# Optimization experiments

Measured on AMD Instinct MI355X. Metric: run time of the kernel, lower is better.

Reference implementation:

```python
import jax, jax.numpy as jnp
import numpy as np

NUM_ITERATIONS = 3
NUM_SLOTS = 8
SLOT_SIZE = 256
MLP_HIDDEN = 512
EPSILON = 1e-8
LN_EPS = 1e-5


def _ln(x, w, b):
    m = jnp.mean(x, axis=-1, keepdims=True)
    v = jnp.var(x, axis=-1, keepdims=True)
    return (x - m) * jax.lax.rsqrt(v + LN_EPS) * w + b


def _gru_cell(x, h, w_ih, w_hh, b_ih, b_hh):
    # torch.nn.GRUCell semantics; gates ordered [r, z, n]
    gi = x @ w_ih.T + b_ih
    gh = h @ w_hh.T + b_hh
    ir, iz, inn = jnp.split(gi, 3, axis=-1)
    hr, hz, hn = jnp.split(gh, 3, axis=-1)
    r = jax.nn.sigmoid(ir + hr)
    z = jax.nn.sigmoid(iz + hz)
    n = jnp.tanh(inn + r * hn)
    return (1.0 - z) * n + z * h


def setup_inputs() -> dict:
    key = jax.random.key(0)
    ks = jax.random.split(key, 12)
    D, H = SLOT_SIZE, MLP_HIDDEN
    s = 0.02
    return {
        "inputs": jax.random.normal(ks[0], (64, 4096, D), dtype=jnp.float32),
        "noise": jax.random.normal(ks[1], (64, NUM_SLOTS, D), dtype=jnp.float32),
        "ln_in_w": jnp.ones((D,), jnp.float32), "ln_in_b": jnp.zeros((D,), jnp.float32),
        "ln_slots_w": jnp.ones((D,), jnp.float32), "ln_slots_b": jnp.zeros((D,), jnp.float32),
        "ln_mlp_w": jnp.ones((D,), jnp.float32), "ln_mlp_b": jnp.zeros((D,), jnp.float32),
        "slots_mu": jax.random.normal(ks[2], (1, 1, D), jnp.float32) * s,
        "slots_log_sigma": jnp.zeros((1, 1, D), jnp.float32),
        "Wq": jax.random.normal(ks[3], (D, D), jnp.float32) * s,
        "Wk": jax.random.normal(ks[4], (D, D), jnp.float32) * s,
        "Wv": jax.random.normal(ks[5], (D, D), jnp.float32) * s,
        "gru_w_ih": jax.random.normal(ks[6], (3 * D, D), jnp.float32) * s,
        "gru_w_hh": jax.random.normal(ks[7], (3 * D, D), jnp.float32) * s,
        "gru_b_ih": jnp.zeros((3 * D,), jnp.float32),
        "gru_b_hh": jnp.zeros((3 * D,), jnp.float32),
        "mlp_w1": jax.random.normal(ks[8], (H, D), jnp.float32) * s,
        "mlp_b1": jnp.zeros((H,), jnp.float32),
        "mlp_w2": jax.random.normal(ks[9], (D, H), jnp.float32) * s,
        "mlp_b2": jnp.zeros((D,), jnp.float32),
    }


def reference(inputs, noise, ln_in_w, ln_in_b, ln_slots_w, ln_slots_b, ln_mlp_w, ln_mlp_b,
              slots_mu, slots_log_sigma, Wq, Wk, Wv,
              gru_w_ih, gru_w_hh, gru_b_ih, gru_b_hh,
              mlp_w1, mlp_b1, mlp_w2, mlp_b2):
    B, N, D = inputs.shape
    S = NUM_SLOTS
    x = _ln(inputs, ln_in_w, ln_in_b)            # [B,N,D]
    k = x @ Wk.T                                  # [B,N,D]
    v = x @ Wv.T                                  # [B,N,D]
    slots = slots_mu + jnp.exp(slots_log_sigma) * noise   # [B,S,D]
    scale = D ** (-0.5)
    for _ in range(NUM_ITERATIONS):
        slots_prev = slots
        s_n = _ln(slots, ln_slots_w, ln_slots_b)
        q = (s_n @ Wq.T) * scale                  # [B,S,D]
        attn_logits = jnp.einsum('bnd,bsd->bns', k, q)
        attn = jax.nn.softmax(attn_logits, axis=-1) + EPSILON
        attn = attn / jnp.sum(attn, axis=-2, keepdims=True)   # renorm over inputs
        updates = jnp.einsum('bns,bnd->bsd', attn, v)          # [B,S,D]
        slots = _gru_cell(updates.reshape(-1, D), slots_prev.reshape(-1, D),
                          gru_w_ih, gru_w_hh, gru_b_ih, gru_b_hh).reshape(B, S, D)
        h = jax.nn.relu(_ln(slots, ln_mlp_w, ln_mlp_b) @ mlp_w1.T + mlp_b1)
        slots = slots + (h @ mlp_w2.T + mlp_b2)
    return slots
```

## Files before the change

kernel.cpp:

```cpp
#include <hip/hip_runtime.h>

#define CB 64
#define CN 4096
#define CD 256
#define CS 8
#define CH 512

typedef __bf16 bf16_t;
typedef bf16_t bf16x8 __attribute__((ext_vector_type(8)));
typedef float f32x4 __attribute__((ext_vector_type(4)));

__device__ __forceinline__ unsigned short f2bf(float f){
  unsigned int u = __builtin_bit_cast(unsigned int, f);
  u += 0x7FFFu + ((u >> 16) & 1u);
  return (unsigned short)(u >> 16);
}

__device__ __forceinline__ f32x4 mfma16(bf16x8 a, bf16x8 b, f32x4 c){
  return __builtin_amdgcn_mfma_f32_16x16x32_bf16(a, b, c, 0, 0, 0);
}

__device__ __forceinline__ void gl_lds16(const void* g, void* l){
  __builtin_amdgcn_global_load_lds(
      (const __attribute__((address_space(1))) unsigned int*)g,
      (__attribute__((address_space(3))) unsigned int*)l, 16, 0, 0);
}

__global__ __launch_bounds__(256) void k_ln(const float* __restrict__ in,
    const float* __restrict__ gw, const float* __restrict__ gb,
    unsigned short* __restrict__ x){
  int blk = blockIdx.x;
  int b = blk >> 6, nt = blk & 63;
  int wv = threadIdx.x >> 6, l = threadIdx.x & 63;
  const float* base = in + ((size_t)b*CN + (size_t)nt*64) * CD;
  unsigned short* xb = x + ((size_t)b*CN + (size_t)nt*64) * CD;
  float4 w4 = *(const float4*)(gw + 4*l);
  float4 b4 = *(const float4*)(gb + 4*l);
  for(int i = 0; i < 16; i++){
    int r = wv*16 + i;
    float4 v = *(const float4*)(base + (size_t)r*CD + 4*l);
    float s1 = v.x + v.y + v.z + v.w;
    float s2 = v.x*v.x + v.y*v.y + v.z*v.z + v.w*v.w;
    #pragma unroll
    for(int m = 1; m < 64; m <<= 1){ s1 += __shfl_xor(s1, m); s2 += __shfl_xor(s2, m); }
    float mean = s1 * (1.0f/CD);
    float var  = fmaxf(s2 * (1.0f/CD) - mean*mean, 0.0f);
    float rstd = rsqrtf(var + 1e-5f);
    float y0 = (v.x - mean)*rstd*w4.x + b4.x;
    float y1 = (v.y - mean)*rstd*w4.y + b4.y;
    float y2 = (v.z - mean)*rstd*w4.z + b4.z;
    float y3 = (v.w - mean)*rstd*w4.w + b4.w;
    uint2 p;
    p.x = (unsigned)f2bf(y0) | ((unsigned)f2bf(y1) << 16);
    p.y = (unsigned)f2bf(y2) | ((unsigned)f2bf(y3) << 16);
    *(uint2*)(xb + (size_t)r*CD + 4*l) = p;
  }
}

__global__ __launch_bounds__(256) void k_setup(
    const float* __restrict__ Wq, const float* __restrict__ Wk,
    const float* __restrict__ wih, const float* __restrict__ Wv,
    const float* __restrict__ whh, const float* __restrict__ w1,
    const float* __restrict__ w2, const float* __restrict__ noise,
    const float* __restrict__ mu, const float* __restrict__ lsig,
    unsigned short* __restrict__ M1T, unsigned short* __restrict__ Mih_bf,
    unsigned short* __restrict__ Whh_bf, unsigned short* __restrict__ w1_bf,
    unsigned short* __restrict__ w2_bf, float* __restrict__ slots){
  int bid = blockIdx.x, tid = threadIdx.x;
  if(bid < 256){
    int ep = bid, e = tid;
    float acc = 0.0f;
    for(int d = 0; d < 256; d++) acc = fmaf(Wq[(size_t)d*256 + e], Wk[(size_t)d*256 + ep], acc);
    M1T[(size_t)ep*256 + e] = f2bf(acc * 0.0625f);
  } else if(bid < 1024){
    int j = bid - 256, e = tid;
    float acc = 0.0f;
    for(int d = 0; d < 256; d++) acc = fmaf(wih[(size_t)j*256 + d], Wv[(size_t)d*256 + e], acc);
    Mih_bf[(size_t)j*256 + e] = f2bf(acc);
  } else if(bid < 1792){
    int idx = (bid - 1024)*256 + tid;
    Whh_bf[idx] = f2bf(whh[idx]);
  } else if(bid < 2304){
    int idx = (bid - 1792)*256 + tid;
    w1_bf[idx] = f2bf(w1[idx]);
  } else if(bid < 2816){
    int idx = (bid - 2304)*256 + tid;
    w2_bf[idx] = f2bf(w2[idx]);
  } else {
    int idx = (bid - 2816)*256 + tid;
    int d = idx & 255;
    slots[idx] = mu[d] + __expf(lsig[d]) * noise[idx];
  }
}

__global__ __launch_bounds__(256) void k_qt(const float* __restrict__ slots,
    const float* __restrict__ lw, const float* __restrict__ lb,
    const unsigned short* __restrict__ M1T, unsigned short* __restrict__ qt,
    float* __restrict__ U, float* __restrict__ den){
  __shared__ unsigned short sn[16*264];
  int b = blockIdx.x;
  int tid = threadIdx.x;
  float4 z4 = {0.f, 0.f, 0.f, 0.f};
  float* Ub = U + (size_t)b*CS*CD;
  *(float4*)(Ub + tid*8)     = z4;
  *(float4*)(Ub + tid*8 + 4) = z4;
  if(tid < CS) den[b*CS + tid] = 0.0f;

  int wv = tid >> 6, l = tid & 63;
  int lm = l & 15, lg = l >> 4;
  float4 w4 = *(const float4*)(lw + 4*l);
  float4 b4 = *(const float4*)(lb + 4*l);
  for(int i = 0; i < 2; i++){
    int r = wv*2 + i;
    float4 v = *(const float4*)(slots + ((size_t)b*CS + r)*CD + 4*l);
    float s1 = v.x + v.y + v.z + v.w;
    float s2 = v.x*v.x + v.y*v.y + v.z*v.z + v.w*v.w;
    #pragma unroll
    for(int m = 1; m < 64; m <<= 1){ s1 += __shfl_xor(s1, m); s2 += __shfl_xor(s2, m); }
    float mean = s1 * (1.0f/CD);
    float var  = fmaxf(s2 * (1.0f/CD) - mean*mean, 0.0f);
    float rstd = rsqrtf(var + 1e-5f);
    float y0 = (v.x - mean)*rstd*w4.x + b4.x;
    float y1 = (v.y - mean)*rstd*w4.y + b4.y;
    float y2 = (v.z - mean)*rstd*w4.z + b4.z;
    float y3 = (v.w - mean)*rstd*w4.w + b4.w;
    uint2 p;
    p.x = (unsigned)f2bf(y0) | ((unsigned)f2bf(y1) << 16);
    p.y = (unsigned)f2bf(y2) | ((unsigned)f2bf(y3) << 16);
    *(uint2*)(&sn[r*264 + 4*l]) = p;
    uint2 zz; zz.x = 0u; zz.y = 0u;
    *(uint2*)(&sn[(r+8)*264 + 4*l]) = zz;
  }
  __syncthreads();
  bf16x8 af[8];
  #pragma unroll
  for(int k = 0; k < 8; k++) af[k] = *(const bf16x8*)(&sn[lm*264 + k*32 + lg*8]);
  #pragma unroll
  for(int ntile = 0; ntile < 4; ntile++){
    int ep = wv*64 + ntile*16 + lm;
    f32x4 acc = {0.f, 0.f, 0.f, 0.f};
    const unsigned short* mrow = M1T + (size_t)ep*CD;
    #pragma unroll
    for(int k = 0; k < 8; k++){
      bf16x8 bf = *(const bf16x8*)(mrow + k*32 + lg*8);
      acc = mfma16(af[k], bf, acc);
    }
    #pragma unroll
    for(int reg = 0; reg < 4; reg++){
      int s = lg*4 + reg;
      qt[((size_t)b*16 + s)*CD + ep] = f2bf(acc[reg]);
    }
  }
}

__global__ __launch_bounds__(256) void k_attn(const unsigned short* __restrict__ x,
    const unsigned short* __restrict__ qt, float* __restrict__ U, float* __restrict__ den){
  __shared__ unsigned short xt[64*256];
  __shared__ unsigned short pt[16*72];
  int b = blockIdx.x >> 4, chunk = blockIdx.x & 15;
  int wv = threadIdx.x >> 6, l = threadIdx.x & 63;
  int lm = l & 15, lg = l >> 4;

  bf16x8 qb[8];
  const unsigned short* qrow = qt + ((size_t)b*16 + lm)*CD;
  #pragma unroll
  for(int k = 0; k < 8; k++) qb[k] = *(const bf16x8*)(qrow + k*32 + lg*8);

  f32x4 uacc[4];
  #pragma unroll
  for(int nt = 0; nt < 4; nt++){ f32x4 z = {0.f,0.f,0.f,0.f}; uacc[nt] = z; }
  float dacc = 0.0f;

  const unsigned short* xbatch = x + (size_t)b*CN*CD + (size_t)chunk*256*CD;

  for(int t = 0; t < 4; t++){
    const unsigned short* xtile = xbatch + (size_t)t*64*CD;
    __syncthreads();
    #pragma unroll
    for(int k2 = 0; k2 < 8; k2++){
      int r0 = wv*16 + k2*2;
      int row = r0 + (l >> 5);
      int c = l & 31;
      int f = (row ^ (row >> 3)) & 7;
      const unsigned short* g = xtile + (size_t)row*CD + (size_t)(c ^ f)*8;
      gl_lds16(g, &xt[r0*CD]);
    }
    __syncthreads();

    f32x4 c4 = {0.f, 0.f, 0.f, 0.f};
    int rowl = wv*16 + lm;
    int f1 = (rowl ^ (rowl >> 3)) & 7;
    #pragma unroll
    for(int k = 0; k < 8; k++){
      int cc = (k*4 + lg) ^ f1;
      bf16x8 a = *(const bf16x8*)(&xt[rowl*256 + cc*8]);
      c4 = mfma16(a, qb[k], c4);
    }
    float pv[4];
    #pragma unroll
    for(int reg = 0; reg < 4; reg++){
      float v = (lm < 8) ? c4[reg] : -1e30f;
      float mx = v;
      #pragma unroll
      for(int m = 1; m < 16; m <<= 1) mx = fmaxf(mx, __shfl_xor(mx, m));
      float e = __expf(v - mx);
      float s = e;
      #pragma unroll
      for(int m = 1; m < 16; m <<= 1) s += __shfl_xor(s, m);
      float p = (lm < 8) ? (e/s + 1e-8f) : 0.0f;
      dacc += p;
      pv[reg] = p;
    }
    int rbase = wv*16 + lg*4;
    unsigned int p01 = (unsigned)f2bf(pv[0]) | ((unsigned)f2bf(pv[1]) << 16);
    unsigned int p23 = (unsigned)f2bf(pv[2]) | ((unsigned)f2bf(pv[3]) << 16);
    *(unsigned int*)(&pt[lm*72 + rbase])     = p01;
    *(unsigned int*)(&pt[lm*72 + rbase + 2]) = p23;
    __syncthreads();

    #pragma unroll
    for(int ks = 0; ks < 2; ks++){
      bf16x8 a = *(const bf16x8*)(&pt[lm*72 + ks*32 + lg*8]);
      int rb = ks*32 + lg*8;
      #pragma unroll
      for(int nt = 0; nt < 4; nt++){
        int e = wv*64 + nt*16 + lm;
        bf16x8 bfr;
        #pragma unroll
        for(int j = 0; j < 8; j++){
          int row2 = rb + j;
          int f2 = (row2 ^ (row2 >> 3)) & 7;
          int cidx = (e >> 3) ^ f2;
          unsigned short tv = xt[row2*256 + cidx*8 + (e & 7)];
          bfr[j] = __builtin_bit_cast(bf16_t, tv);
        }
        uacc[nt] = mfma16(a, bfr, uacc[nt]);
      }
    }
  }

  dacc += __shfl_xor(dacc, 16);
  dacc += __shfl_xor(dacc, 32);
  if(l < 8) atomicAdd(&den[b*CS + l], dacc);
  if(lg < 2){
    #pragma unroll
    for(int nt = 0; nt < 4; nt++){
      #pragma unroll
      for(int reg = 0; reg < 4; reg++){
        int s = lg*4 + reg;
        atomicAdd(&U[((size_t)b*CS + s)*CD + wv*64 + nt*16 + lm], uacc[nt][reg]);
      }
    }
  }
}

__global__ __launch_bounds__(256) void k_update(
    const float* __restrict__ U, const float* slots,
    const float* __restrict__ den,
    const unsigned short* __restrict__ Mih, const unsigned short* __restrict__ Whh,
    const unsigned short* __restrict__ w1b, const unsigned short* __restrict__ w2b,
    const unsigned short* __restrict__ M1T,
    const float* __restrict__ bih, const float* __restrict__ bhh,
    const float* __restrict__ lmw, const float* __restrict__ lmb,
    const float* __restrict__ b1, const float* __restrict__ b2,
    const float* __restrict__ lsw, const float* __restrict__ lsb,
    float* out, unsigned short* __restrict__ qt,
    float* __restrict__ Uz, float* __restrict__ denz, int last){
  __shared__ unsigned short A1[16*264];
  __shared__ unsigned short SBf[16*264];
  __shared__ unsigned short A3[16*520];
  __shared__ float G1[8*777];
  __shared__ float G2[8*777];
  __shared__ float Hh[8*257];
  __shared__ float SN[8*257];
  int b = blockIdx.x, tid = threadIdx.x;
  int l = tid & 63, lm = l & 15, lg = l >> 4;
  int wv = tid >> 6;

  for(int i = tid; i < 8*264; i += 256){ A1[8*264 + i] = 0; SBf[8*264 + i] = 0; }
  for(int i = tid; i < 8*520; i += 256) A3[8*520 + i] = 0;
  {
    int r = tid >> 5, c = (tid & 31)*8;
    const float* Ur = U + ((size_t)b*CS + r)*CD + c;
    float4 a0 = *(const float4*)Ur, a1 = *(const float4*)(Ur + 4);
    uint4 pk;
    pk.x = (unsigned)f2bf(a0.x) | ((unsigned)f2bf(a0.y) << 16);
    pk.y = (unsigned)f2bf(a0.z) | ((unsigned)f2bf(a0.w) << 16);
    pk.z = (unsigned)f2bf(a1.x) | ((unsigned)f2bf(a1.y) << 16);
    pk.w = (unsigned)f2bf(a1.z) | ((unsigned)f2bf(a1.w) << 16);
    *(uint4*)(&A1[r*264 + c]) = pk;
    const float* Sr = slots + ((size_t)b*CS + r)*CD + c;
    a0 = *(const float4*)Sr; a1 = *(const float4*)(Sr + 4);
    pk.x = (unsigned)f2bf(a0.x) | ((unsigned)f2bf(a0.y) << 16);
    pk.y = (unsigned)f2bf(a0.z) | ((unsigned)f2bf(a0.w) << 16);
    pk.z = (unsigned)f2bf(a1.x) | ((unsigned)f2bf(a1.y) << 16);
    pk.w = (unsigned)f2bf(a1.z) | ((unsigned)f2bf(a1.w) << 16);
    *(uint4*)(&SBf[r*264 + c]) = pk;
  }
  __syncthreads();

  {
    bf16x8 afU[8], afS[8];
    #pragma unroll
    for(int k = 0; k < 8; k++){
      afU[k] = *(const bf16x8*)(&A1[lm*264 + k*32 + lg*8]);
      afS[k] = *(const bf16x8*)(&SBf[lm*264 + k*32 + lg*8]);
    }
    for(int t = 0; t < 12; t++){
      int nb = wv*192 + t*16;
      const unsigned short* br1 = Mih + (size_t)(nb + lm)*CD;
      const unsigned short* br2 = Whh + (size_t)(nb + lm)*CD;
      f32x4 ac1 = {0.f,0.f,0.f,0.f}, ac2 = {0.f,0.f,0.f,0.f};
      #pragma unroll
      for(int k = 0; k < 8; k++){
        bf16x8 bv1 = *(const bf16x8*)(br1 + k*32 + lg*8);
        ac1 = mfma16(afU[k], bv1, ac1);
        bf16x8 bv2 = *(const bf16x8*)(br2 + k*32 + lg*8);
        ac2 = mfma16(afS[k], bv2, ac2);
      }
      if(lg < 2){
        #pragma unroll
        for(int reg = 0; reg < 4; reg++){
          int row = lg*4 + reg;
          G1[row*777 + nb + lm] = ac1[reg];
          G2[row*777 + nb + lm] = ac2[reg];
        }
      }
    }
  }
  __syncthreads();

  {
    int r = tid >> 5, cl = tid & 31;
    float invd = 1.0f / den[b*CS + r];
    const float* srow = slots + ((size_t)b*CS + r)*CD;
    float hv[8]; float s1 = 0.f, s2 = 0.f;
    #pragma unroll
    for(int i = 0; i < 8; i++){
      int c = cl + 32*i;
      float gr = G1[r*777 + c]*invd + bih[c] + G2[r*777 + c] + bhh[c];
      float gz = G1[r*777 + 256 + c]*invd + bih[256 + c] + G2[r*777 + 256 + c] + bhh[256 + c];
      float gn = G1[r*777 + 512 + c]*invd + bih[512 + c];
      float hn = G2[r*777 + 512 + c] + bhh[512 + c];
      float rr = 1.0f/(1.0f + __expf(-gr));
      float zz = 1.0f/(1.0f + __expf(-gz));
      float nn = tanhf(gn + rr*hn);
      float h = (1.0f - zz)*nn + zz*srow[c];
      hv[i] = h; Hh[r*257 + c] = h; s1 += h; s2 += h*h;
    }
    #pragma unroll
    for(int m = 1; m < 32; m <<= 1){ s1 += __shfl_xor(s1, m); s2 += __shfl_xor(s2, m); }
    float mean = s1 * (1.0f/CD);
    float var  = fmaxf(s2 * (1.0f/CD) - mean*mean, 0.0f);
    float rstd = rsqrtf(var + 1e-5f);
    #pragma unroll
    for(int i = 0; i < 8; i++){
      int c = cl + 32*i;
      A1[r*264 + c] = f2bf((hv[i] - mean)*rstd*lmw[c] + lmb[c]);
    }
  }
  __syncthreads();

  {
    bf16x8 af[8];
    #pragma unroll
    for(int k = 0; k < 8; k++) af[k] = *(const bf16x8*)(&A1[lm*264 + k*32 + lg*8]);
    for(int t = 0; t < 8; t++){
      int nb = wv*128 + t*16;
      const unsigned short* br = w1b + (size_t)(nb + lm)*CD;
      f32x4 acc = {0.f,0.f,0.f,0.f};
      #pragma unroll
      for(int k = 0; k < 8; k++){
        bf16x8 bv = *(const bf16x8*)(br + k*32 + lg*8);
        acc = mfma16(af[k], bv, acc);
      }
      if(lg < 2){
        int c = nb + lm;
        float bb = b1[c];
        #pragma unroll
        for(int reg = 0; reg < 4; reg++)
          A3[(lg*4 + reg)*520 + c] = f2bf(fmaxf(acc[reg] + bb, 0.0f));
      }
    }
  }
  __syncthreads();

  {
    bf16x8 af[16];
    #pragma unroll
    for(int k = 0; k < 16; k++) af[k] = *(const bf16x8*)(&A3[lm*520 + k*32 + lg*8]);
    for(int t = 0; t < 4; t++){
      int nb = wv*64 + t*16;
      const unsigned short* br = w2b + (size_t)(nb + lm)*CH;
      f32x4 acc = {0.f,0.f,0.f,0.f};
      #pragma unroll
      for(int k = 0; k < 16; k++){
        bf16x8 bv = *(const bf16x8*)(br + k*32 + lg*8);
        acc = mfma16(af[k], bv, acc);
      }
      if(lg < 2){
        int c = nb + lm;
        float bb = b2[c];
        #pragma unroll
        for(int reg = 0; reg < 4; reg++){
          int row = lg*4 + reg;
          float v = acc[reg] + bb + Hh[row*257 + c];
          out[((size_t)b*CS + row)*CD + c] = v;
          SN[row*257 + c] = v;
        }
      }
    }
  }
  if(last) return;
  __syncthreads();

  {
    int r = tid >> 5, cl = tid & 31;
    float sv[8]; float s1 = 0.f, s2 = 0.f;
    #pragma unroll
    for(int i = 0; i < 8; i++){
      int c = cl + 32*i;
      float v = SN[r*257 + c]; sv[i] = v; s1 += v; s2 += v*v;
    }
    #pragma unroll
    for(int m = 1; m < 32; m <<= 1){ s1 += __shfl_xor(s1, m); s2 += __shfl_xor(s2, m); }
    float mean = s1 * (1.0f/CD);
    float var  = fmaxf(s2 * (1.0f/CD) - mean*mean, 0.0f);
    float rstd = rsqrtf(var + 1e-5f);
    #pragma unroll
    for(int i = 0; i < 8; i++){
      int c = cl + 32*i;
      A1[r*264 + c] = f2bf((sv[i] - mean)*rstd*lsw[c] + lsb[c]);
    }
  }
  __syncthreads();
  {
    bf16x8 af[8];
    #pragma unroll
    for(int k = 0; k < 8; k++) af[k] = *(const bf16x8*)(&A1[lm*264 + k*32 + lg*8]);
    for(int t = 0; t < 4; t++){
      int nb = wv*64 + t*16;
      const unsigned short* br = M1T + (size_t)(nb + lm)*CD;
      f32x4 acc = {0.f,0.f,0.f,0.f};
      #pragma unroll
      for(int k = 0; k < 8; k++){
        bf16x8 bv = *(const bf16x8*)(br + k*32 + lg*8);
        acc = mfma16(af[k], bv, acc);
      }
      if(lg < 2){
        int c = nb + lm;
        #pragma unroll
        for(int reg = 0; reg < 4; reg++)
          qt[((size_t)b*16 + lg*4 + reg)*CD + c] = f2bf(acc[reg]);
      }
    }
  }
  {
    float4 z4 = {0.f,0.f,0.f,0.f};
    float* Ub = Uz + (size_t)b*CS*CD;
    *(float4*)(Ub + tid*8)     = z4;
    *(float4*)(Ub + tid*8 + 4) = z4;
    if(tid < CS) denz[b*CS + tid] = 0.0f;
  }
}

extern "C" void kernel_launch(void* const* d_in, const int* in_sizes, int n_in,
                              void* d_out, int out_size, void* d_ws, size_t ws_size,
                              hipStream_t stream){
  const float* inputs = (const float*)d_in[0];
  const float* noise  = (const float*)d_in[1];
  const float* ln_in_w = (const float*)d_in[2];
  const float* ln_in_b = (const float*)d_in[3];
  const float* ln_sl_w = (const float*)d_in[4];
  const float* ln_sl_b = (const float*)d_in[5];
  const float* ln_ml_w = (const float*)d_in[6];
  const float* ln_ml_b = (const float*)d_in[7];
  const float* mu   = (const float*)d_in[8];
  const float* lsig = (const float*)d_in[9];
  const float* Wq  = (const float*)d_in[10];
  const float* Wk  = (const float*)d_in[11];
  const float* Wv  = (const float*)d_in[12];
  const float* wih = (const float*)d_in[13];
  const float* whh = (const float*)d_in[14];
  const float* bih = (const float*)d_in[15];
  const float* bhh = (const float*)d_in[16];
  const float* w1  = (const float*)d_in[17];
  const float* b1  = (const float*)d_in[18];
  const float* w2  = (const float*)d_in[19];
  const float* b2  = (const float*)d_in[20];

  char* ws = (char*)d_ws;
  size_t off = 0;
  unsigned short* x = (unsigned short*)(ws + off); off += (size_t)CB*CN*CD*2;
  float* slots = (float*)(ws + off); off += (size_t)CB*CS*CD*4;
  float* U     = (float*)(ws + off); off += (size_t)CB*CS*CD*4;
  float* den   = (float*)(ws + off); off += (size_t)CB*CS*4;
  unsigned short* qt     = (unsigned short*)(ws + off); off += (size_t)CB*16*CD*2;
  unsigned short* M1T    = (unsigned short*)(ws + off); off += (size_t)CD*CD*2;
  unsigned short* Mih_bf = (unsigned short*)(ws + off); off += (size_t)768*CD*2;
  unsigned short* Whh_bf = (unsigned short*)(ws + off); off += (size_t)768*CD*2;
  unsigned short* w1_bf  = (unsigned short*)(ws + off); off += (size_t)CH*CD*2;
  unsigned short* w2_bf  = (unsigned short*)(ws + off); off += (size_t)CD*CH*2;

  k_ln<<<4096, 256, 0, stream>>>(inputs, ln_in_w, ln_in_b, x);
  k_setup<<<3328, 256, 0, stream>>>(Wq, Wk, wih, Wv, whh, w1, w2, noise, mu, lsig,
                                    M1T, Mih_bf, Whh_bf, w1_bf, w2_bf, slots);
  k_qt<<<64, 256, 0, stream>>>(slots, ln_sl_w, ln_sl_b, M1T, qt, U, den);

  for(int it = 0; it < 3; it++){
    k_attn<<<1024, 256, 0, stream>>>(x, qt, U, den);
    float* dst = (it == 2) ? (float*)d_out : slots;
    k_update<<<64, 256, 0, stream>>>(U, slots, den,
        Mih_bf, Whh_bf, w1_bf, w2_bf, M1T,
        bih, bhh, ln_ml_w, ln_ml_b, b1, b2, ln_sl_w, ln_sl_b,
        dst, qt, U, den, (it == 2) ? 1 : 0);
  }
}
```

Baseline: 711.0 us.

## Widen k_update to 512 threads, split GRU GEMMs per wave, unfuse q-projection

Doubles k_update to 512 threads. Waves 0-3 now compute the input-side GRU GEMM and waves 4-7 the hidden-side GEMM, with a register double-buffer that prefetches the next weight tile. The slot-LN, q-projection and U/den zeroing tail moves out of k_update, and k_qt is launched at the start of every iteration instead of once. The goal is more parallelism and latency hiding in the small 64-block update kernel, at the cost of two extra kernel launches and re-reading slots from global memory in k_qt.

```diff
diff --git a/kernel.cpp b/kernel.cpp
--- a/kernel.cpp
+++ b/kernel.cpp
@@ -254,90 +254,82 @@
   }
 }
 
-__global__ __launch_bounds__(256) void k_update(
+__global__ __launch_bounds__(512) void k_update(
     const float* __restrict__ U, const float* slots,
     const float* __restrict__ den,
     const unsigned short* __restrict__ Mih, const unsigned short* __restrict__ Whh,
     const unsigned short* __restrict__ w1b, const unsigned short* __restrict__ w2b,
-    const unsigned short* __restrict__ M1T,
     const float* __restrict__ bih, const float* __restrict__ bhh,
     const float* __restrict__ lmw, const float* __restrict__ lmb,
     const float* __restrict__ b1, const float* __restrict__ b2,
-    const float* __restrict__ lsw, const float* __restrict__ lsb,
-    float* out, unsigned short* __restrict__ qt,
-    float* __restrict__ Uz, float* __restrict__ denz, int last){
+    float* out){
   __shared__ unsigned short A1[16*264];
   __shared__ unsigned short SBf[16*264];
   __shared__ unsigned short A3[16*520];
   __shared__ float G1[8*777];
   __shared__ float G2[8*777];
   __shared__ float Hh[8*257];
-  __shared__ float SN[8*257];
   int b = blockIdx.x, tid = threadIdx.x;
   int l = tid & 63, lm = l & 15, lg = l >> 4;
   int wv = tid >> 6;
 
-  for(int i = tid; i < 8*264; i += 256){ A1[8*264 + i] = 0; SBf[8*264 + i] = 0; }
-  for(int i = tid; i < 8*520; i += 256) A3[8*520 + i] = 0;
+  for(int i = tid; i < 8*264; i += 512){ A1[8*264 + i] = 0; SBf[8*264 + i] = 0; }
+  for(int i = tid; i < 8*520; i += 512) A3[8*520 + i] = 0;
   {
-    int r = tid >> 5, c = (tid & 31)*8;
-    const float* Ur = U + ((size_t)b*CS + r)*CD + c;
-    float4 a0 = *(const float4*)Ur, a1 = *(const float4*)(Ur + 4);
+    int t2 = tid & 255;
+    int r = t2 >> 5, c = (t2 & 31)*8;
+    const float* src = ((tid < 256) ? U : slots) + ((size_t)b*CS + r)*CD + c;
+    float4 a0 = *(const float4*)src, a1 = *(const float4*)(src + 4);
     uint4 pk;
     pk.x = (unsigned)f2bf(a0.x) | ((unsigned)f2bf(a0.y) << 16);
     pk.y = (unsigned)f2bf(a0.z) | ((unsigned)f2bf(a0.w) << 16);
     pk.z = (unsigned)f2bf(a1.x) | ((unsigned)f2bf(a1.y) << 16);
     pk.w = (unsigned)f2bf(a1.z) | ((unsigned)f2bf(a1.w) << 16);
-    *(uint4*)(&A1[r*264 + c]) = pk;
-    const float* Sr = slots + ((size_t)b*CS + r)*CD + c;
-    a0 = *(const float4*)Sr; a1 = *(const float4*)(Sr + 4);
-    pk.x = (unsigned)f2bf(a0.x) | ((unsigned)f2bf(a0.y) << 16);
-    pk.y = (unsigned)f2bf(a0.z) | ((unsigned)f2bf(a0.w) << 16);
-    pk.z = (unsigned)f2bf(a1.x) | ((unsigned)f2bf(a1.y) << 16);
-    pk.w = (unsigned)f2bf(a1.z) | ((unsigned)f2bf(a1.w) << 16);
-    *(uint4*)(&SBf[r*264 + c]) = pk;
+    if(tid < 256) *(uint4*)(&A1[r*264 + c]) = pk;
+    else          *(uint4*)(&SBf[r*264 + c]) = pk;
   }
   __syncthreads();
 
   {
-    bf16x8 afU[8], afS[8];
-    #pragma unroll
-    for(int k = 0; k < 8; k++){
-      afU[k] = *(const bf16x8*)(&A1[lm*264 + k*32 + lg*8]);
-      afS[k] = *(const bf16x8*)(&SBf[lm*264 + k*32 + lg*8]);
-    }
+    const unsigned short* W = (wv < 4) ? Mih : Whh;
+    const unsigned short* As = (wv < 4) ? A1 : SBf;
+    float* G = (wv < 4) ? G1 : G2;
+    int w4 = wv & 3;
+    bf16x8 af[8];
+    #pragma unroll
+    for(int k = 0; k < 8; k++) af[k] = *(const bf16x8*)(&As[lm*264 + k*32 + lg*8]);
+    const unsigned short* brow = W + ((size_t)(w4*192 + lm))*CD + lg*8;
+    bf16x8 bv[8], bw[8];
+    #pragma unroll
+    for(int k = 0; k < 8; k++) bv[k] = *(const bf16x8*)(brow + k*32);
     for(int t = 0; t < 12; t++){
-      int nb = wv*192 + t*16;
-      const unsigned short* br1 = Mih + (size_t)(nb + lm)*CD;
-      const unsigned short* br2 = Whh + (size_t)(nb + lm)*CD;
-      f32x4 ac1 = {0.f,0.f,0.f,0.f}, ac2 = {0.f,0.f,0.f,0.f};
-      #pragma unroll
-      for(int k = 0; k < 8; k++){
-        bf16x8 bv1 = *(const bf16x8*)(br1 + k*32 + lg*8);
-        ac1 = mfma16(afU[k], bv1, ac1);
-        bf16x8 bv2 = *(const bf16x8*)(br2 + k*32 + lg*8);
-        ac2 = mfma16(afS[k], bv2, ac2);
-      }
+      if(t < 11){
+        const unsigned short* bn = brow + (size_t)(t + 1)*16*CD;
+        #pragma unroll
+        for(int k = 0; k < 8; k++) bw[k] = *(const bf16x8*)(bn + k*32);
+      }
+      f32x4 acc = {0.f,0.f,0.f,0.f};
+      #pragma unroll
+      for(int k = 0; k < 8; k++) acc = mfma16(af[k], bv[k], acc);
       if(lg < 2){
+        int cb = w4*192 + t*16 + lm;
         #pragma unroll
-        for(int reg = 0; reg < 4; reg++){
-          int row = lg*4 + reg;
-          G1[row*777 + nb + lm] = ac1[reg];
-          G2[row*777 + nb + lm] = ac2[reg];
-        }
-      }
+        for(int reg = 0; reg < 4; reg++) G[(lg*4 + reg)*777 + cb] = acc[reg];
+      }
+      #pragma unroll
+      for(int k = 0; k < 8; k++) bv[k] = bw[k];
     }
   }
   __syncthreads();
 
   {
-    int r = tid >> 5, cl = tid & 31;
+    int r = wv;
     float invd = 1.0f / den[b*CS + r];
     const float* srow = slots + ((size_t)b*CS + r)*CD;
-    float hv[8]; float s1 = 0.f, s2 = 0.f;
-    #pragma unroll
-    for(int i = 0; i < 8; i++){
-      int c = cl + 32*i;
+    float hv[4]; float s1 = 0.f, s2 = 0.f;
+    #pragma unroll
+    for(int i = 0; i < 4; i++){
+      int c = l + 64*i;
       float gr = G1[r*777 + c]*invd + bih[c] + G2[r*777 + c] + bhh[c];
       float gz = G1[r*777 + 256 + c]*invd + bih[256 + c] + G2[r*777 + 256 + c] + bhh[256 + c];
       float gn = G1[r*777 + 512 + c]*invd + bih[512 + c];
@@ -349,13 +341,13 @@
       hv[i] = h; Hh[r*257 + c] = h; s1 += h; s2 += h*h;
     }
     #pragma unroll
-    for(int m = 1; m < 32; m <<= 1){ s1 += __shfl_xor(s1, m); s2 += __shfl_xor(s2, m); }
+    for(int m = 1; m < 64; m <<= 1){ s1 += __shfl_xor(s1, m); s2 += __shfl_xor(s2, m); }
     float mean = s1 * (1.0f/CD);
     float var  = fmaxf(s2 * (1.0f/CD) - mean*mean, 0.0f);
     float rstd = rsqrtf(var + 1e-5f);
     #pragma unroll
-    for(int i = 0; i < 8; i++){
-      int c = cl + 32*i;
+    for(int i = 0; i < 4; i++){
+      int c = l + 64*i;
       A1[r*264 + c] = f2bf((hv[i] - mean)*rstd*lmw[c] + lmb[c]);
     }
   }
@@ -365,17 +357,17 @@
     bf16x8 af[8];
     #pragma unroll
     for(int k = 0; k < 8; k++) af[k] = *(const bf16x8*)(&A1[lm*264 + k*32 + lg*8]);
-    for(int t = 0; t < 8; t++){
-      int nb = wv*128 + t*16;
-      const unsigned short* br = w1b + (size_t)(nb + lm)*CD;
+    const unsigned short* brow = w1b + ((size_t)(wv*64 + lm))*CD + lg*8;
+    for(int t = 0; t < 4; t++){
+      const unsigned short* bn = brow + (size_t)t*16*CD;
       f32x4 acc = {0.f,0.f,0.f,0.f};
       #pragma unroll
       for(int k = 0; k < 8; k++){
-        bf16x8 bv = *(const bf16x8*)(br + k*32 + lg*8);
+        bf16x8 bv = *(const bf16x8*)(bn + k*32);
         acc = mfma16(af[k], bv, acc);
       }
       if(lg < 2){
-        int c = nb + lm;
+        int c = wv*64 + t*16 + lm;
         float bb = b1[c];
         #pragma unroll
         for(int reg = 0; reg < 4; reg++)
@@ -389,78 +381,25 @@
     bf16x8 af[16];
     #pragma unroll
     for(int k = 0; k < 16; k++) af[k] = *(const bf16x8*)(&A3[lm*520 + k*32 + lg*8]);
-    for(int t = 0; t < 4; t++){
-      int nb = wv*64 + t*16;
-      const unsigned short* br = w2b + (size_t)(nb + lm)*CH;
+    const unsigned short* brow = w2b + ((size_t)(wv*32 + lm))*CH + lg*8;
+    for(int t = 0; t < 2; t++){
+      const unsigned short* bn = brow + (size_t)t*16*CH;
       f32x4 acc = {0.f,0.f,0.f,0.f};
       #pragma unroll
       for(int k = 0; k < 16; k++){
-        bf16x8 bv = *(const bf16x8*)(br + k*32 + lg*8);
+        bf16x8 bv = *(const bf16x8*)(bn + k*32);
         acc = mfma16(af[k], bv, acc);
       }
       if(lg < 2){
-        int c = nb + lm;
+        int c = wv*32 + t*16 + lm;
         float bb = b2[c];
         #pragma unroll
         for(int reg = 0; reg < 4; reg++){
           int row = lg*4 + reg;
-          float v = acc[reg] + bb + Hh[row*257 + c];
-          out[((size_t)b*CS + row)*CD + c] = v;
-          SN[row*257 + c] = v;
+          out[((size_t)b*CS + row)*CD + c] = acc[reg] + bb + Hh[row*257 + c];
         }
       }
     }
-  }
-  if(last) return;
-  __syncthreads();
-
-  {
-    int r = tid >> 5, cl = tid & 31;
-    float sv[8]; float s1 = 0.f, s2 = 0.f;
-    #pragma unroll
-    for(int i = 0; i < 8; i++){
-      int c = cl + 32*i;
-      float v = SN[r*257 + c]; sv[i] = v; s1 += v; s2 += v*v;
-    }
-    #pragma unroll
-    for(int m = 1; m < 32; m <<= 1){ s1 += __shfl_xor(s1, m); s2 += __shfl_xor(s2, m); }
-    float mean = s1 * (1.0f/CD);
-    float var  = fmaxf(s2 * (1.0f/CD) - mean*mean, 0.0f);
-    float rstd = rsqrtf(var + 1e-5f);
-    #pragma unroll
-    for(int i = 0; i < 8; i++){
-      int c = cl + 32*i;
-      A1[r*264 + c] = f2bf((sv[i] - mean)*rstd*lsw[c] + lsb[c]);
-    }
-  }
-  __syncthreads();
-  {
-    bf16x8 af[8];
-    #pragma unroll
-    for(int k = 0; k < 8; k++) af[k] = *(const bf16x8*)(&A1[lm*264 + k*32 + lg*8]);
-    for(int t = 0; t < 4; t++){
-      int nb = wv*64 + t*16;
-      const unsigned short* br = M1T + (size_t)(nb + lm)*CD;
-      f32x4 acc = {0.f,0.f,0.f,0.f};
-      #pragma unroll
-      for(int k = 0; k < 8; k++){
-        bf16x8 bv = *(const bf16x8*)(br + k*32 + lg*8);
-        acc = mfma16(af[k], bv, acc);
-      }
-      if(lg < 2){
-        int c = nb + lm;
-        #pragma unroll
-        for(int reg = 0; reg < 4; reg++)
-          qt[((size_t)b*16 + lg*4 + reg)*CD + c] = f2bf(acc[reg]);
-      }
-    }
-  }
-  {
-    float4 z4 = {0.f,0.f,0.f,0.f};
-    float* Ub = Uz + (size_t)b*CS*CD;
-    *(float4*)(Ub + tid*8)     = z4;
-    *(float4*)(Ub + tid*8 + 4) = z4;
-    if(tid < CS) denz[b*CS + tid] = 0.0f;
   }
 }
 
@@ -505,14 +444,13 @@
   k_ln<<<4096, 256, 0, stream>>>(inputs, ln_in_w, ln_in_b, x);
   k_setup<<<3328, 256, 0, stream>>>(Wq, Wk, wih, Wv, whh, w1, w2, noise, mu, lsig,
                                     M1T, Mih_bf, Whh_bf, w1_bf, w2_bf, slots);
-  k_qt<<<64, 256, 0, stream>>>(slots, ln_sl_w, ln_sl_b, M1T, qt, U, den);
 
   for(int it = 0; it < 3; it++){
+    k_qt<<<64, 256, 0, stream>>>(slots, ln_sl_w, ln_sl_b, M1T, qt, U, den);
     k_attn<<<1024, 256, 0, stream>>>(x, qt, U, den);
     float* dst = (it == 2) ? (float*)d_out : slots;
-    k_update<<<64, 256, 0, stream>>>(U, slots, den,
-        Mih_bf, Whh_bf, w1_bf, w2_bf, M1T,
-        bih, bhh, ln_ml_w, ln_ml_b, b1, b2, ln_sl_w, ln_sl_b,
-        dst, qt, U, den, (it == 2) ? 1 : 0);
-  }
-}
+    k_update<<<64, 512, 0, stream>>>(U, slots, den,
+        Mih_bf, Whh_bf, w1_bf, w2_bf,
+        bih, bhh, ln_ml_w, ln_ml_b, b1, b2, dst);
+  }
+}
```

New measurement: 684.4 us. 3.7% less time.
